# Kernel optimization log

Hardware: AMD Instinct MI355X
Metric: run time of the kernel (lower is better)

The kernel has to match this reference:

```python
import jax, jax.numpy as jnp
import numpy as np
from jax import lax

B, CO, CI, KH, KW, H, W = 32, 128, 128, 3, 3, 56, 56
STRIDE = (1, 1)
PADDING = ((1, 1), (1, 1))


def setup_inputs() -> dict:
    key = jax.random.key(0)
    k1, k2, k3, k4 = jax.random.split(key, 4)
    inp = jax.random.normal(k1, (B, CI, H, W), dtype=jnp.float32)
    eps = jax.random.normal(k2, (B, CO, CI, KH, KW), dtype=jnp.float32)
    # reset_parameters: psi ~ U(-6, -5); mu ~ U(-stdv, stdv), stdv = 1/sqrt(CI*KH*KW)
    weight_psi = jax.random.uniform(k3, (CO, CI, KH, KW), dtype=jnp.float32,
                                    minval=-6.0, maxval=-5.0)
    stdv = 1.0 / np.sqrt(CI * KH * KW)
    weight_mu = jax.random.uniform(k4, (CO, CI, KH, KW), dtype=jnp.float32,
                                   minval=-stdv, maxval=stdv)
    return {"input": inp, "eps": eps, "weight_psi": weight_psi, "weight_mu": weight_mu}


def reference(input, eps, weight_psi, weight_mu):
    # mul_exp_add: per-sample weight = eps * exp(psi) + mu  -> [B, CO, CI, KH, KW]
    weight = eps * jnp.exp(weight_psi) + weight_mu

    # Per-example conv (torch does it via groups = bs trick); here vmap over batch.
    def conv_one(x, w):  # x: [CI,H,W], w: [CO,CI,KH,KW]
        return lax.conv_general_dilated(
            x[None], w, window_strides=STRIDE, padding=PADDING,
            dimension_numbers=("NCHW", "OIHW", "NCHW"))[0]

    out = jax.vmap(conv_one)(input, weight)  # [B, CO, H, W]
    return out
```

## Files before the change

### kernel.cpp

```cpp
#include <hip/hip_runtime.h>
#include <hip/hip_bf16.h>

#define CO    128
#define CI    128
#define NPIX  3136
#define PH    58
#define PPIX  3364
#define HPX   232
#define SROW  272

typedef __bf16 bf16x8 __attribute__((ext_vector_type(8)));
typedef float  f32x4  __attribute__((ext_vector_type(4)));

__global__ void prep_all(const float* __restrict__ in,
                         const float* __restrict__ eps,
                         const float* __restrict__ psi,
                         const float* __restrict__ mu,
                         __bf16* __restrict__ wt,
                         __bf16* __restrict__ it) {
  __shared__ __align__(16) __bf16 T[64][136];
  const int bx = blockIdx.x, tid = threadIdx.x;

  if (bx < 2048) {
    int idx = bx * 256 + tid;
    int ci = idx & 127;
    int co = (idx >> 7) & 127;
    const float* e  = eps + (size_t)idx * 9;
    const float* ps = psi + (size_t)(co * CI + ci) * 9;
    const float* m  = mu  + (size_t)(co * CI + ci) * 9;
    float v[9];
#pragma unroll
    for (int p = 0; p < 9; ++p) v[p] = e[p] * __expf(ps[p]) + m[p];
    int b = idx >> 14;
    __bf16* w = wt + ((size_t)b * 9 * CO + co) * CI + ci;
#pragma unroll
    for (int p = 0; p < 9; ++p) w[(size_t)p * CO * CI] = (__bf16)v[p];
  } else if (bx < 2504) {
    int cid = (bx - 2048) * 256 + tid;
    int pid = cid >> 4;
    int chunk = cid & 15;
    int b = pid / 228;
    int e = pid - b * 228;
    int ph, pw;
    if (e < 58)       { ph = 0;       pw = e; }
    else if (e < 116) { ph = 57;      pw = e - 58; }
    else if (e < 172) { ph = e - 115; pw = 0; }
    else              { ph = e - 171; pw = 57; }
    f32x4 z = {0.f, 0.f, 0.f, 0.f};
    *(f32x4*)&it[((size_t)b * PPIX + ph * PH + pw) * CI + chunk * 8] = z;
  } else {
    int tx = bx - 2504;
    int b  = tx / 49;
    int p0 = (tx - b * 49) * 64;
    const float* src = in + (size_t)b * CI * NPIX;
#pragma unroll
    for (int jj = 0; jj < 8; ++jj) {
      int c = jj * 256 + tid;
      int ci = c >> 4, xc = c & 15;
      float4 v = *(const float4*)(src + (size_t)ci * NPIX + p0 + xc * 4);
      T[xc * 4 + 0][ci] = (__bf16)v.x;
      T[xc * 4 + 1][ci] = (__bf16)v.y;
      T[xc * 4 + 2][ci] = (__bf16)v.z;
      T[xc * 4 + 3][ci] = (__bf16)v.w;
    }
    __syncthreads();
    __bf16* dstb = it + (size_t)b * PPIX * CI;
#pragma unroll
    for (int jj = 0; jj < 4; ++jj) {
      int c = jj * 256 + tid;
      int pl = c >> 4, xc = c & 15;
      int pix = p0 + pl;
      int oh = pix / 56, ow = pix - oh * 56;
      int ppix = (oh + 1) * PH + (ow + 1);
      *(f32x4*)&dstb[(size_t)ppix * CI + xc * 8] = *(const f32x4*)&T[pl][xc * 8];
    }
  }
}

__global__ __launch_bounds__(256) void bconv_gemm(
    const __bf16* __restrict__ wt,
    const __bf16* __restrict__ it,
    float* __restrict__ out) {
  __shared__ __align__(16) char Bsh[HPX * SROW];
  const int tid  = threadIdx.x;
  const int w    = tid >> 6;
  const int lane = tid & 63;
  const int quad = lane >> 4;
  const int l15  = lane & 15;

  const int lin = blockIdx.x;
  const int x   = lin & 7;
  const int j   = lin >> 3;
  const int bhi = j & 3;
  const int tile = j >> 2;
  const int b   = x + 8 * bhi;
  const int oh0 = tile * 2;

  const __bf16* hsrc = it + ((size_t)b * PPIX + oh0 * PH) * CI;
#pragma unroll
  for (int i = 0; i < 15; ++i) {
    int idx = i * 256 + tid;
    if (idx < HPX * 16) {
      int px = idx >> 4, sub = idx & 15;
      f32x4 v = *(const f32x4*)(hsrc + (size_t)idx * 8);
      *(f32x4*)&Bsh[px * SROW + sub * 16] = v;
    }
  }
  __syncthreads();

  int bbase[7];
#pragma unroll
  for (int nf = 0; nf < 7; ++nf) {
    int n = nf * 16 + l15;
    int r = (n >= 56) ? 1 : 0;
    int c = n - r * 56;
    bbase[nf] = (r * PH + c) * SROW + quad * 16;
  }

  const int co0 = w * 32;
  const __bf16* wtb = wt + (size_t)b * 9 * CO * CI;
  const int ab0 = (co0 +      l15) * CI + quad * 8;
  const int ab1 = (co0 + 16 + l15) * CI + quad * 8;

  f32x4 acc[2][7] = {};
  bf16x8 acur[2], anxt[2];
  acur[0] = *(const bf16x8*)(wtb + ab0);
  acur[1] = *(const bf16x8*)(wtb + ab1);

#pragma unroll
  for (int s = 0; s < 36; ++s) {
    const int p   = s >> 2;
    const int ci0 = (s & 3) << 5;
    if (s < 35) {
      const int pn   = (s + 1) >> 2;
      const int ci0n = ((s + 1) & 3) << 5;
      const __bf16* ap = wtb + pn * (CO * CI) + ci0n;
      anxt[0] = *(const bf16x8*)(ap + ab0);
      anxt[1] = *(const bf16x8*)(ap + ab1);
    }
    const int kh = p / 3, kw = p - kh * 3;
    const int tapb = (kh * PH + kw) * SROW + ci0 * 2;
#pragma unroll
    for (int nf = 0; nf < 7; ++nf) {
      bf16x8 bfr = *(const bf16x8*)&Bsh[bbase[nf] + tapb];
      acc[0][nf] = __builtin_amdgcn_mfma_f32_16x16x32_bf16(acur[0], bfr, acc[0][nf], 0, 0, 0);
      acc[1][nf] = __builtin_amdgcn_mfma_f32_16x16x32_bf16(acur[1], bfr, acc[1][nf], 0, 0, 0);
    }
    acur[0] = anxt[0];
    acur[1] = anxt[1];
  }

  float* ob = out + (size_t)b * CO * NPIX + oh0 * 56;
#pragma unroll
  for (int mf = 0; mf < 2; ++mf) {
#pragma unroll
    for (int nf = 0; nf < 7; ++nf) {
#pragma unroll
      for (int r = 0; r < 4; ++r) {
        int co = co0 + mf * 16 + quad * 4 + r;
        ob[(size_t)co * NPIX + nf * 16 + l15] = acc[mf][nf][r];
      }
    }
  }
}

extern "C" void kernel_launch(void* const* d_in, const int* in_sizes, int n_in,
                              void* d_out, int out_size, void* d_ws, size_t ws_size,
                              hipStream_t stream) {
  const float* inp = (const float*)d_in[0];
  const float* eps = (const float*)d_in[1];
  const float* psi = (const float*)d_in[2];
  const float* mu  = (const float*)d_in[3];

  __bf16* wt = (__bf16*)d_ws;
  __bf16* it = (__bf16*)((char*)d_ws + 9437184);

  prep_all<<<4072, 256, 0, stream>>>(inp, eps, psi, mu, wt, it);
  bconv_gemm<<<896, 256, 0, stream>>>(wt, it, (float*)d_out);
}
```

Measured before the change: 159.4 us.

## Use 2 waves per block with 64-row CO tiles and double-buffered A/B fragments

Halves the block size to 128 threads, so each wave now covers 64 output channels (4 M-fragments) instead of 32, which doubles reuse of each LDS B fragment across MFMAs. The main loop now double-buffers both the global A loads and the LDS B loads, so loads for step s+1 are issued before the MFMAs of step s. The halo copy loop is resized for 128 threads. In exchange, each wave holds 112 accumulator registers plus doubled fragment buffers, which raises register pressure, and the smaller block with launch_bounds(128,1) may lower occupancy and latency hiding.

Result: slower. 166.7 us (+4.6%).

```diff
diff --git a/kernel.cpp b/kernel.cpp
--- a/kernel.cpp
+++ b/kernel.cpp
@@ -77,7 +77,36 @@
   }
 }
 
-__global__ __launch_bounds__(256) void bconv_gemm(
+__device__ __forceinline__ void loadB(const char* Bsh, const int* bbase, int tapb,
+                                      bf16x8 bf[7]) {
+#pragma unroll
+  for (int nf = 0; nf < 7; ++nf)
+    bf[nf] = *(const bf16x8*)&Bsh[bbase[nf] + tapb];
+}
+
+__device__ __forceinline__ void loadA(const __bf16* wtb, const int* ab, int s,
+                                      bf16x8 af[4]) {
+  const int p   = s >> 2;
+  const int ci0 = (s & 3) << 5;
+  const __bf16* ap = wtb + p * (CO * CI) + ci0;
+#pragma unroll
+  for (int mf = 0; mf < 4; ++mf)
+    af[mf] = *(const bf16x8*)(ap + ab[mf]);
+}
+
+__device__ __forceinline__ void do_mfma(const bf16x8 af[4], const bf16x8 bf[7],
+                                        f32x4 acc[4][7]) {
+#pragma unroll
+  for (int mf = 0; mf < 4; ++mf)
+#pragma unroll
+    for (int nf = 0; nf < 7; ++nf)
+      acc[mf][nf] = __builtin_amdgcn_mfma_f32_16x16x32_bf16(
+          af[mf], bf[nf], acc[mf][nf], 0, 0, 0);
+}
+
+#define TAPB(s) ((((s) >> 2) / 3) * PH + (((s) >> 2) % 3)) * SROW + (((s) & 3) << 6)
+
+__global__ __launch_bounds__(128, 1) void bconv_gemm(
     const __bf16* __restrict__ wt,
     const __bf16* __restrict__ it,
     float* __restrict__ out) {
@@ -98,13 +127,11 @@
 
   const __bf16* hsrc = it + ((size_t)b * PPIX + oh0 * PH) * CI;
 #pragma unroll
-  for (int i = 0; i < 15; ++i) {
-    int idx = i * 256 + tid;
-    if (idx < HPX * 16) {
-      int px = idx >> 4, sub = idx & 15;
-      f32x4 v = *(const f32x4*)(hsrc + (size_t)idx * 8);
-      *(f32x4*)&Bsh[px * SROW + sub * 16] = v;
-    }
+  for (int i = 0; i < 29; ++i) {
+    int idx = i * 128 + tid;
+    int px = idx >> 4, sub = idx & 15;
+    f32x4 v = *(const f32x4*)(hsrc + (size_t)idx * 8);
+    *(f32x4*)&Bsh[px * SROW + sub * 16] = v;
   }
   __syncthreads();
 
@@ -113,46 +140,38 @@
   for (int nf = 0; nf < 7; ++nf) {
     int n = nf * 16 + l15;
     int r = (n >= 56) ? 1 : 0;
-    int c = n - r * 56;
-    bbase[nf] = (r * PH + c) * SROW + quad * 16;
+    bbase[nf] = (n + 2 * r) * SROW + quad * 16;
   }
 
-  const int co0 = w * 32;
+  const int co0 = w * 64;
   const __bf16* wtb = wt + (size_t)b * 9 * CO * CI;
-  const int ab0 = (co0 +      l15) * CI + quad * 8;
-  const int ab1 = (co0 + 16 + l15) * CI + quad * 8;
+  int ab[4];
+#pragma unroll
+  for (int mf = 0; mf < 4; ++mf)
+    ab[mf] = (co0 + mf * 16 + l15) * CI + quad * 8;
 
-  f32x4 acc[2][7] = {};
-  bf16x8 acur[2], anxt[2];
-  acur[0] = *(const bf16x8*)(wtb + ab0);
-  acur[1] = *(const bf16x8*)(wtb + ab1);
+  f32x4 acc[4][7] = {};
+  bf16x8 a0[4], a1[4], b0[7], b1[7];
 
+  loadA(wtb, ab, 0, a0);
+  loadB(Bsh, bbase, TAPB(0), b0);
 #pragma unroll
-  for (int s = 0; s < 36; ++s) {
-    const int p   = s >> 2;
-    const int ci0 = (s & 3) << 5;
-    if (s < 35) {
-      const int pn   = (s + 1) >> 2;
-      const int ci0n = ((s + 1) & 3) << 5;
-      const __bf16* ap = wtb + pn * (CO * CI) + ci0n;
-      anxt[0] = *(const bf16x8*)(ap + ab0);
-      anxt[1] = *(const bf16x8*)(ap + ab1);
-    }
-    const int kh = p / 3, kw = p - kh * 3;
-    const int tapb = (kh * PH + kw) * SROW + ci0 * 2;
-#pragma unroll
-    for (int nf = 0; nf < 7; ++nf) {
-      bf16x8 bfr = *(const bf16x8*)&Bsh[bbase[nf] + tapb];
-      acc[0][nf] = __builtin_amdgcn_mfma_f32_16x16x32_bf16(acur[0], bfr, acc[0][nf], 0, 0, 0);
-      acc[1][nf] = __builtin_amdgcn_mfma_f32_16x16x32_bf16(acur[1], bfr, acc[1][nf], 0, 0, 0);
-    }
-    acur[0] = anxt[0];
-    acur[1] = anxt[1];
+  for (int s = 0; s < 34; s += 2) {
+    loadA(wtb, ab, s + 1, a1);
+    loadB(Bsh, bbase, TAPB(s + 1), b1);
+    do_mfma(a0, b0, acc);
+    loadA(wtb, ab, s + 2, a0);
+    loadB(Bsh, bbase, TAPB(s + 2), b0);
+    do_mfma(a1, b1, acc);
   }
+  loadA(wtb, ab, 35, a1);
+  loadB(Bsh, bbase, TAPB(35), b1);
+  do_mfma(a0, b0, acc);
+  do_mfma(a1, b1, acc);
 
   float* ob = out + (size_t)b * CO * NPIX + oh0 * 56;
 #pragma unroll
-  for (int mf = 0; mf < 2; ++mf) {
+  for (int mf = 0; mf < 4; ++mf) {
 #pragma unroll
     for (int nf = 0; nf < 7; ++nf) {
 #pragma unroll
@@ -176,5 +195,5 @@
   __bf16* it = (__bf16*)((char*)d_ws + 9437184);
 
   prep_all<<<4072, 256, 0, stream>>>(inp, eps, psi, mu, wt, it);
-  bconv_gemm<<<896, 256, 0, stream>>>(wt, it, (float*)d_out);
+  bconv_gemm<<<896, 128, 0, stream>>>(wt, it, (float*)d_out);
 }
```
